# Kernel optimization log

Measured on AMD Instinct MI355X. Metric: run time of the kernel, lower is better.

The kernel has to match this reference:

```python
import jax, jax.numpy as jnp
import numpy as np

D_MODEL = 768
D_HEAD = 64
N_HEADS = D_MODEL // D_HEAD


def setup_inputs() -> dict:
    key = jax.random.key(0)
    k1, k2, k3 = jax.random.split(key, 3)
    n, h, w = 2, 48, 48
    x = jax.random.normal(k1, (n, h, w, D_MODEL), dtype=jnp.float32)
    # torch Linear weights: [out_features, in_features]
    w_qkv = jax.random.normal(k2, (3 * D_MODEL, D_MODEL), dtype=jnp.float32) * (D_MODEL ** -0.5)
    w_out = jax.random.normal(k3, (D_MODEL, D_MODEL), dtype=jnp.float32) * (D_MODEL ** -0.5)
    return {"x": x, "w_qkv": w_qkv, "w_out": w_out, "kernel_size": 7}


def _natten_mask(h: int, w: int, kernel_size: int) -> jnp.ndarray:
    # Faithful to _natten_mask_mod: q_x = idx // w, q_y = idx % w,
    # both axes compared against the same kernel_size.
    idx = jnp.arange(h * w)
    qx, qy = idx // w, idx % w
    horiz = jnp.abs(qx[:, None] - qx[None, :]) <= kernel_size
    vert = jnp.abs(qy[:, None] - qy[None, :]) <= kernel_size
    return horiz & vert  # [hw, hw] bool


def reference(x, w_qkv, w_out, kernel_size):
    n, h, w, d = x.shape
    hw = h * w
    qkv = jnp.einsum('nhwd,fd->nhwf', x, w_qkv)  # [n, h, w, 3*d]
    qkv = qkv.reshape(n, hw, 3, N_HEADS, D_HEAD)
    q = jnp.transpose(qkv[:, :, 0], (0, 2, 1, 3))  # [n, nh, hw, e]
    k = jnp.transpose(qkv[:, :, 1], (0, 2, 1, 3))
    v = jnp.transpose(qkv[:, :, 2], (0, 2, 1, 3))

    mask = _natten_mask(h, w, kernel_size)  # [hw, hw]
    scale = D_HEAD ** -0.5
    scores = jnp.einsum('bnqe,bnke->bnqk', q, k) * scale
    neg = jnp.asarray(jnp.finfo(scores.dtype).min, scores.dtype)
    scores = jnp.where(mask[None, None], scores, neg)
    attn = jax.nn.softmax(scores, axis=-1)
    o = jnp.einsum('bnqk,bnke->bnqe', attn, v)  # [n, nh, hw, e]
    o = jnp.transpose(o, (0, 2, 1, 3)).reshape(n, h, w, d)
    return jnp.einsum('nhwd,fd->nhwf', o, w_out)
```

## Files before the change

kernel.cpp:

```cpp
#include <hip/hip_runtime.h>

using f32x4 = __attribute__((ext_vector_type(4))) float;
using h8v   = __attribute__((ext_vector_type(8))) _Float16;
using h4v   = __attribute__((ext_vector_type(4))) _Float16;
using s8v   = __attribute__((ext_vector_type(8))) short;

#define MFMAH(a, b, c)   __builtin_amdgcn_mfma_f32_16x16x32_f16((a), (b), (c), 0, 0, 0)
#define MFMAH16(a, b, c) __builtin_amdgcn_mfma_f32_16x16x16f16((a), (b), (c), 0, 0, 0)

typedef __attribute__((address_space(3))) unsigned int lds_uint;
typedef const __attribute__((address_space(1))) unsigned int glb_uint;
__device__ inline void gload16(void* l, const void* g) {
    __builtin_amdgcn_global_load_lds((glb_uint*)g, (lds_uint*)l, 16, 0, 0);
}

__device__ inline float exp2_fast(float x) {
    float r;
    asm("v_exp_f32 %0, %1" : "=v"(r) : "v"(x));
    return r;
}

__global__ __launch_bounds__(256) void conv_all(const float* __restrict__ x,
                                                const float* __restrict__ wq,
                                                const float* __restrict__ wo,
                                                _Float16* __restrict__ xh,
                                                _Float16* __restrict__ wqh,
                                                _Float16* __restrict__ woh) {
    const int i = blockIdx.x * blockDim.x + threadIdx.x;
    const float* src;
    _Float16* dst;
    int off;
    if (i < 442368)      { src = x;  dst = xh;  off = i; }
    else if (i < 663552) { src = wq; dst = wqh; off = i - 442368; }
    else                 { src = wo; dst = woh; off = i - 663552; }
    const float4 a = *(const float4*)(src + (size_t)off * 8);
    const float4 b = *(const float4*)(src + (size_t)off * 8 + 4);
    h8v h;
    h[0] = (_Float16)a.x; h[1] = (_Float16)a.y; h[2] = (_Float16)a.z; h[3] = (_Float16)a.w;
    h[4] = (_Float16)b.x; h[5] = (_Float16)b.y; h[6] = (_Float16)b.z; h[7] = (_Float16)b.w;
    *(h8v*)(dst + (size_t)off * 8) = h;
}

__global__ __launch_bounds__(256) void gemm_qkv_f16(const _Float16* __restrict__ A,
                                                    const _Float16* __restrict__ B,
                                                    _Float16* __restrict__ C) {
    constexpr int LD = 768, LDC = 2304;
    __shared__ __align__(16) _Float16 sA[128][64], sB[128][64];
    const int b = blockIdx.x;
    const int sb = (b & 7) * 81 + (b >> 3);
    const int bx = sb % 18, by = sb / 18;
    const int m0 = by * 128, n0 = bx * 128;
    const int tid = threadIdx.x, lane = tid & 63, wv = tid >> 6;
    const int wm = (wv >> 1) * 64, wn = (wv & 1) * 64;
    const int fr = lane & 15, fkb = (lane >> 4) * 8;

    const int srow = tid >> 3, scol = (tid & 7) * 8;
    const _Float16* gA = A + (size_t)(m0 + srow) * LD + scol;
    const _Float16* gB = B + (size_t)(n0 + srow) * LD + scol;

    f32x4 acc[4][4];
#pragma unroll
    for (int m = 0; m < 4; ++m)
#pragma unroll
        for (int n2 = 0; n2 < 4; ++n2) acc[m][n2] = (f32x4){0.f, 0.f, 0.f, 0.f};

    for (int kt = 0; kt < 12; ++kt) {
        const int k0 = kt * 64;
#pragma unroll
        for (int q = 0; q < 4; ++q) {
            gload16(&sA[q * 32 + srow][scol], gA + (size_t)(q * 32) * LD + k0);
            gload16(&sB[q * 32 + srow][scol], gB + (size_t)(q * 32) * LD + k0);
        }
        __syncthreads();

#pragma unroll
        for (int kk = 0; kk < 2; ++kk) {
            h8v fa[4], fb[4];
#pragma unroll
            for (int m = 0; m < 4; ++m) fa[m] = *(const h8v*)&sA[wm + m * 16 + fr][kk * 32 + fkb];
#pragma unroll
            for (int n2 = 0; n2 < 4; ++n2) fb[n2] = *(const h8v*)&sB[wn + n2 * 16 + fr][kk * 32 + fkb];
#pragma unroll
            for (int m = 0; m < 4; ++m)
#pragma unroll
                for (int n2 = 0; n2 < 4; ++n2) acc[m][n2] = MFMAH(fa[m], fb[n2], acc[m][n2]);
        }
        __syncthreads();
    }

    const int rg = (lane >> 4) * 4;
#pragma unroll
    for (int m = 0; m < 4; ++m)
#pragma unroll
        for (int n2 = 0; n2 < 4; ++n2)
#pragma unroll
            for (int r = 0; r < 4; ++r)
                C[(size_t)(m0 + wm + m * 16 + rg + r) * LDC + (n0 + wn + n2 * 16 + fr)] =
                    (_Float16)acc[m][n2][r];
}

__global__ __launch_bounds__(256) void vtrans(const unsigned short* __restrict__ qkv,
                                              unsigned short* __restrict__ vt) {
    __shared__ unsigned short t[64][72];
    const int tt = blockIdx.x, head = blockIdx.y, n = blockIdx.z;
    const int tid = threadIdx.x;
#pragma unroll
    for (int i = 0; i < 2; ++i) {
        const int el = i * 2048 + tid * 8;
        const int tr = el >> 6, c = el & 63;
        s8v v = *(const s8v*)(qkv + (size_t)(n * 2304 + tt * 64 + tr) * 2304 + 1536 + head * 64 + c);
        *(s8v*)&t[tr][c] = v;
    }
    __syncthreads();
#pragma unroll
    for (int i = 0; i < 2; ++i) {
        const int el = i * 2048 + tid * 8;
        const int er = el >> 6, tk = el & 63;
        s8v w;
#pragma unroll
        for (int j = 0; j < 8; ++j) w[j] = (short)t[tk + j][er];
        *(s8v*)(vt + (size_t)((n * 12 + head) * 64 + er) * 2304 + tt * 64 + tk) = w;
    }
}

__global__ __launch_bounds__(192) void attn_flash(const _Float16* __restrict__ qkv,
                                                  const _Float16* __restrict__ vt,
                                                  _Float16* __restrict__ o,
                                                  const int* __restrict__ ksp) {
    __shared__ __align__(16) char sbuf[2][14336];
    const int tid = threadIdx.x;
    const int lane = tid & 63, wv = tid >> 6;
    const int fr = lane & 15, fg = lane >> 4;

    const int b = blockIdx.x;
    const int xcd = b & 7, g = b >> 3;
    const int qx = xcd * 6 + g / 24;
    const int hn = g % 24;
    const int head = hn >> 1, n = hn & 1;
    const int KS = *ksp;

    const int krow0 = tid >> 3, kc = tid & 7;
    const int vrow0 = tid / 6,  vc = tid % 6;
    const int ksw = (krow0 & 7) << 4;
    const int vsw = (vrow0 & 7) << 4;

    const int qy = wv * 16 + fr;
    const _Float16* qrow = qkv + (size_t)(n * 2304 + qx * 48 + qy) * 2304 + head * 64;
    h8v qa0 = *(const h8v*)(qrow + fg * 8);
    h8v qa1 = *(const h8v*)(qrow + 32 + fg * 8);
    qa0 = qa0 * (_Float16)0.1803368801f;
    qa1 = qa1 * (_Float16)0.1803368801f;

    int nt0 = (wv * 16 - KS) >> 4;      if (nt0 < 0) nt0 = 0;
    int nt1 = (wv * 16 + 15 + KS) >> 4; if (nt1 > 2) nt1 = 2;

    f32x4 mbias[3];
#pragma unroll
    for (int nt = 0; nt < 3; ++nt)
#pragma unroll
        for (int r = 0; r < 4; ++r) {
            const int dy = nt * 16 + fg * 4 + r - qy;
            mbias[nt][r] = (dy < -KS || dy > KS) ? -1e4f : 0.f;
        }

    f32x4 Oacc[4];
#pragma unroll
    for (int e = 0; e < 4; ++e) Oacc[e] = (f32x4){0.f, 0.f, 0.f, 0.f};
    float rs_acc = 0.f;

    const int lo = (qx - KS) > 0 ? (qx - KS) : 0;
    const int hi = (qx + KS) < 47 ? (qx + KS) : 47;

    const _Float16* kgbase = qkv + (size_t)(n * 2304) * 2304 + 768 + head * 64;
    const _Float16* vgbase = vt + (size_t)((n * 12 + head) * 64) * 2304;

    {
        const _Float16* kg = kgbase + (size_t)(lo * 48) * 2304;
        const _Float16* vg = vgbase + lo * 48;
        const s8v a0 = *(const s8v*)(kg + (size_t)krow0 * 2304 + kc * 8);
        const s8v a1 = *(const s8v*)(kg + (size_t)(krow0 + 24) * 2304 + kc * 8);
        const s8v b0 = *(const s8v*)(vg + (size_t)vrow0 * 2304 + vc * 8);
        const s8v b1 = *(const s8v*)(vg + (size_t)(vrow0 + 32) * 2304 + vc * 8);
        *(s8v*)(sbuf[0] + krow0 * 128 + ((kc * 16) ^ ksw)) = a0;
        *(s8v*)(sbuf[0] + (krow0 + 24) * 128 + ((kc * 16) ^ ksw)) = a1;
        *(s8v*)(sbuf[0] + 6144 + vrow0 * 128 + ((vc * 16) ^ vsw)) = b0;
        *(s8v*)(sbuf[0] + 6144 + (vrow0 + 32) * 128 + ((vc * 16) ^ vsw)) = b1;
    }

    int p = 0;
    for (int kx = lo; kx <= hi; ++kx) {
        __syncthreads();
        const bool pre = (kx < hi);
        s8v tk0, tk1, tv0, tv1;
        if (pre) {
            const _Float16* kg = kgbase + (size_t)((kx + 1) * 48) * 2304;
            const _Float16* vg = vgbase + (kx + 1) * 48;
            tk0 = *(const s8v*)(kg + (size_t)krow0 * 2304 + kc * 8);
            tk1 = *(const s8v*)(kg + (size_t)(krow0 + 24) * 2304 + kc * 8);
            tv0 = *(const s8v*)(vg + (size_t)vrow0 * 2304 + vc * 8);
            tv1 = *(const s8v*)(vg + (size_t)(vrow0 + 32) * 2304 + vc * 8);
        }

        const char* K = sbuf[p];
        const char* V = sbuf[p] + 6144;

        f32x4 s[3];
#pragma unroll
        for (int nt = 0; nt < 3; ++nt)
            if (nt >= nt0 && nt <= nt1) {
                const int rr = nt * 16 + fr;
                const int sw = (rr & 7) << 4;
                const h8v kb0 = *(const h8v*)(K + rr * 128 + ((fg * 16) ^ sw));
                const h8v kb1 = *(const h8v*)(K + rr * 128 + ((64 + fg * 16) ^ sw));
                f32x4 z = MFMAH(kb0, qa0, mbias[nt]);
                z = MFMAH(kb1, qa1, z);
                s[nt] = z;
            }

#pragma unroll
        for (int nt = 0; nt < 3; ++nt)
            if (nt >= nt0 && nt <= nt1) {
                h4v pa;
#pragma unroll
                for (int r = 0; r < 4; ++r) {
                    const float pv = exp2_fast(s[nt][r]);
                    rs_acc += pv;
                    pa[r] = (_Float16)pv;
                }
                const int slot = nt * 2 + (fg >> 1), off8 = (fg & 1) * 8;
#pragma unroll
                for (int et = 0; et < 4; ++et) {
                    const int rv = et * 16 + fr;
                    const h4v vb = *(const h4v*)(V + rv * 128 +
                                                 (((slot ^ (rv & 7)) << 4) + off8));
                    Oacc[et] = MFMAH16(vb, pa, Oacc[et]);
                }
            }

        if (pre) {
            char* d = sbuf[p ^ 1];
            *(s8v*)(d + krow0 * 128 + ((kc * 16) ^ ksw)) = tk0;
            *(s8v*)(d + (krow0 + 24) * 128 + ((kc * 16) ^ ksw)) = tk1;
            *(s8v*)(d + 6144 + vrow0 * 128 + ((vc * 16) ^ vsw)) = tv0;
            *(s8v*)(d + 6144 + (vrow0 + 32) * 128 + ((vc * 16) ^ vsw)) = tv1;
        }
        p ^= 1;
    }

    rs_acc += __shfl_xor(rs_acc, 16);
    rs_acc += __shfl_xor(rs_acc, 32);
    const float linv = 1.f / rs_acc;
    _Float16* ob = o + (size_t)(n * 2304 + qx * 48 + wv * 16 + fr) * 768 + head * 64;
#pragma unroll
    for (int et = 0; et < 4; ++et) {
        h4v ov;
#pragma unroll
        for (int r = 0; r < 4; ++r) ov[r] = (_Float16)(Oacc[et][r] * linv);
        *(h4v*)(ob + et * 16 + fg * 4) = ov;
    }
}

__global__ __launch_bounds__(256) void gemm_out_f16(const _Float16* __restrict__ A,
                                                    const _Float16* __restrict__ B,
                                                    float* __restrict__ C) {
    constexpr int LD = 768, LDC = 768;
    __shared__ __align__(16) _Float16 sA[128][64], sB[128][64];
    const int b = blockIdx.x;
    const int sb = (b & 7) * 27 + (b >> 3);
    const int bx = sb % 6, by = sb / 6;
    const int m0 = by * 128, n0 = bx * 128;
    const int tid = threadIdx.x, lane = tid & 63, wv = tid >> 6;
    const int wm = (wv >> 1) * 64, wn = (wv & 1) * 64;
    const int fr = lane & 15, fkb = (lane >> 4) * 8;

    const int srow = tid >> 3, scol = (tid & 7) * 8;
    const _Float16* gA = A + (size_t)(m0 + srow) * LD + scol;
    const _Float16* gB = B + (size_t)(n0 + srow) * LD + scol;

    f32x4 acc[4][4];
#pragma unroll
    for (int m = 0; m < 4; ++m)
#pragma unroll
        for (int n2 = 0; n2 < 4; ++n2) acc[m][n2] = (f32x4){0.f, 0.f, 0.f, 0.f};

    for (int kt = 0; kt < 12; ++kt) {
        const int k0 = kt * 64;
#pragma unroll
        for (int q = 0; q < 4; ++q) {
            gload16(&sA[q * 32 + srow][scol], gA + (size_t)(q * 32) * LD + k0);
            gload16(&sB[q * 32 + srow][scol], gB + (size_t)(q * 32) * LD + k0);
        }
        __syncthreads();

#pragma unroll
        for (int kk = 0; kk < 2; ++kk) {
            h8v fa[4], fb[4];
#pragma unroll
            for (int m = 0; m < 4; ++m) fa[m] = *(const h8v*)&sA[wm + m * 16 + fr][kk * 32 + fkb];
#pragma unroll
            for (int n2 = 0; n2 < 4; ++n2) fb[n2] = *(const h8v*)&sB[wn + n2 * 16 + fr][kk * 32 + fkb];
#pragma unroll
            for (int m = 0; m < 4; ++m)
#pragma unroll
                for (int n2 = 0; n2 < 4; ++n2) acc[m][n2] = MFMAH(fa[m], fb[n2], acc[m][n2]);
        }
        __syncthreads();
    }

    const int rg = (lane >> 4) * 4;
#pragma unroll
    for (int m = 0; m < 4; ++m)
#pragma unroll
        for (int n2 = 0; n2 < 4; ++n2)
#pragma unroll
            for (int r = 0; r < 4; ++r)
                C[(size_t)(m0 + wm + m * 16 + rg + r) * LDC + (n0 + wn + n2 * 16 + fr)] =
                    acc[m][n2][r];
}

extern "C" void kernel_launch(void* const* d_in, const int* in_sizes, int n_in,
                              void* d_out, int out_size, void* d_ws, size_t ws_size,
                              hipStream_t stream) {
    const float* x     = (const float*)d_in[0];
    const float* w_qkv = (const float*)d_in[1];
    const float* w_out = (const float*)d_in[2];
    const int*   ksp   = (const int*)d_in[3];
    float* out = (float*)d_out;

    char* ws = (char*)d_ws;
    _Float16* qkv = (_Float16*)(ws);
    _Float16* vt  = (_Float16*)(ws + 21237760);
    _Float16* o   = (_Float16*)(ws + 28315648);
    _Float16* xh  = (_Float16*)(ws + 35393536);
    _Float16* wqh = (_Float16*)(ws + 42471424);
    _Float16* woh = (_Float16*)(ws + 46010368);

    conv_all<<<dim3(2880), 256, 0, stream>>>(x, w_qkv, w_out, xh, wqh, woh);
    gemm_qkv_f16<<<dim3(648), 256, 0, stream>>>(xh, wqh, qkv);
    vtrans<<<dim3(36, 12, 2), 256, 0, stream>>>((const unsigned short*)qkv,
                                                (unsigned short*)vt);
    attn_flash<<<dim3(1152), 192, 0, stream>>>(qkv, vt, o, ksp);
    gemm_out_f16<<<dim3(216), 256, 0, stream>>>(o, woh, out);
}
```

Measured before the change: 86.73 us.

## Double-buffer GEMM K-tiles and share K/V loads across two query rows

Both GEMMs switch from a single 64-wide K tile to double-buffered 32-wide tiles, so the global→LDS async load of the next tile overlaps the MFMAs on the current one and one barrier per step is dropped. The attention kernel now uses 384-thread blocks covering two adjacent query rows. Each K/V row tile is loaded once and shared, and each wave skips rows outside its own window. This halves redundant K/V traffic per row pair, at the cost of some idle iterations per wave and larger blocks.

```diff
diff --git a/kernel.cpp b/kernel.cpp
--- a/kernel.cpp
+++ b/kernel.cpp
@@ -45,7 +45,7 @@
                                                     const _Float16* __restrict__ B,
                                                     _Float16* __restrict__ C) {
     constexpr int LD = 768, LDC = 2304;
-    __shared__ __align__(16) _Float16 sA[128][64], sB[128][64];
+    __shared__ __align__(16) _Float16 sA[2][128][32], sB[2][128][32];
     const int b = blockIdx.x;
     const int sb = (b & 7) * 81 + (b >> 3);
     const int bx = sb % 18, by = sb / 18;
@@ -54,7 +54,7 @@
     const int wm = (wv >> 1) * 64, wn = (wv & 1) * 64;
     const int fr = lane & 15, fkb = (lane >> 4) * 8;
 
-    const int srow = tid >> 3, scol = (tid & 7) * 8;
+    const int srow = tid >> 2, scol = (tid & 3) * 8;
     const _Float16* gA = A + (size_t)(m0 + srow) * LD + scol;
     const _Float16* gB = B + (size_t)(n0 + srow) * LD + scol;
 
@@ -64,28 +64,33 @@
 #pragma unroll
         for (int n2 = 0; n2 < 4; ++n2) acc[m][n2] = (f32x4){0.f, 0.f, 0.f, 0.f};
 
-    for (int kt = 0; kt < 12; ++kt) {
-        const int k0 = kt * 64;
-#pragma unroll
-        for (int q = 0; q < 4; ++q) {
-            gload16(&sA[q * 32 + srow][scol], gA + (size_t)(q * 32) * LD + k0);
-            gload16(&sB[q * 32 + srow][scol], gB + (size_t)(q * 32) * LD + k0);
-        }
+    gload16(&sA[0][srow][scol],      gA);
+    gload16(&sA[0][64 + srow][scol], gA + 64 * LD);
+    gload16(&sB[0][srow][scol],      gB);
+    gload16(&sB[0][64 + srow][scol], gB + 64 * LD);
+
+    int cur = 0;
+    for (int kt = 0; kt < 24; ++kt) {
+        asm volatile("s_waitcnt vmcnt(0)" ::: "memory");
         __syncthreads();
-
-#pragma unroll
-        for (int kk = 0; kk < 2; ++kk) {
-            h8v fa[4], fb[4];
-#pragma unroll
-            for (int m = 0; m < 4; ++m) fa[m] = *(const h8v*)&sA[wm + m * 16 + fr][kk * 32 + fkb];
-#pragma unroll
-            for (int n2 = 0; n2 < 4; ++n2) fb[n2] = *(const h8v*)&sB[wn + n2 * 16 + fr][kk * 32 + fkb];
-#pragma unroll
-            for (int m = 0; m < 4; ++m)
-#pragma unroll
-                for (int n2 = 0; n2 < 4; ++n2) acc[m][n2] = MFMAH(fa[m], fb[n2], acc[m][n2]);
-        }
-        __syncthreads();
+        if (kt + 1 < 24) {
+            const int k1 = (kt + 1) * 32;
+            gload16(&sA[cur ^ 1][srow][scol],      gA + k1);
+            gload16(&sA[cur ^ 1][64 + srow][scol], gA + 64 * LD + k1);
+            gload16(&sB[cur ^ 1][srow][scol],      gB + k1);
+            gload16(&sB[cur ^ 1][64 + srow][scol], gB + 64 * LD + k1);
+        }
+
+        h8v fa[4], fb[4];
+#pragma unroll
+        for (int m = 0; m < 4; ++m) fa[m] = *(const h8v*)&sA[cur][wm + m * 16 + fr][fkb];
+#pragma unroll
+        for (int n2 = 0; n2 < 4; ++n2) fb[n2] = *(const h8v*)&sB[cur][wn + n2 * 16 + fr][fkb];
+#pragma unroll
+        for (int m = 0; m < 4; ++m)
+#pragma unroll
+            for (int n2 = 0; n2 < 4; ++n2) acc[m][n2] = MFMAH(fa[m], fb[n2], acc[m][n2]);
+        cur ^= 1;
     }
 
     const int rg = (lane >> 4) * 4;
@@ -123,26 +128,28 @@
     }
 }
 
-__global__ __launch_bounds__(192) void attn_flash(const _Float16* __restrict__ qkv,
+__global__ __launch_bounds__(384) void attn_flash(const _Float16* __restrict__ qkv,
                                                   const _Float16* __restrict__ vt,
                                                   _Float16* __restrict__ o,
                                                   const int* __restrict__ ksp) {
     __shared__ __align__(16) char sbuf[2][14336];
     const int tid = threadIdx.x;
-    const int lane = tid & 63, wv = tid >> 6;
+    const int lane = tid & 63, w = tid >> 6;
     const int fr = lane & 15, fg = lane >> 4;
 
     const int b = blockIdx.x;
     const int xcd = b & 7, g = b >> 3;
-    const int qx = xcd * 6 + g / 24;
+    const int qxp = xcd * 3 + g / 24;
     const int hn = g % 24;
     const int head = hn >> 1, n = hn & 1;
+    const int qxl = w / 3, wv = w % 3;
+    const int qx = qxp * 2 + qxl;
     const int KS = *ksp;
 
-    const int krow0 = tid >> 3, kc = tid & 7;
-    const int vrow0 = tid / 6,  vc = tid % 6;
-    const int ksw = (krow0 & 7) << 4;
-    const int vsw = (vrow0 & 7) << 4;
+    const int krow = tid >> 3, kc = tid & 7;
+    const int vrow = tid / 6,  vc = tid % 6;
+    const int ksw = (krow & 7) << 4;
+    const int vsw = (vrow & 7) << 4;
 
     const int qy = wv * 16 + fr;
     const _Float16* qrow = qkv + (size_t)(n * 2304 + qx * 48 + qy) * 2304 + head * 64;
@@ -168,81 +175,72 @@
     for (int e = 0; e < 4; ++e) Oacc[e] = (f32x4){0.f, 0.f, 0.f, 0.f};
     float rs_acc = 0.f;
 
-    const int lo = (qx - KS) > 0 ? (qx - KS) : 0;
-    const int hi = (qx + KS) < 47 ? (qx + KS) : 47;
+    const int lo = (2 * qxp - KS) > 0 ? (2 * qxp - KS) : 0;
+    const int hi = (2 * qxp + 1 + KS) < 47 ? (2 * qxp + 1 + KS) : 47;
+    const int wlo = qx - KS, whi = qx + KS;
 
     const _Float16* kgbase = qkv + (size_t)(n * 2304) * 2304 + 768 + head * 64;
     const _Float16* vgbase = vt + (size_t)((n * 12 + head) * 64) * 2304;
 
     {
-        const _Float16* kg = kgbase + (size_t)(lo * 48) * 2304;
-        const _Float16* vg = vgbase + lo * 48;
-        const s8v a0 = *(const s8v*)(kg + (size_t)krow0 * 2304 + kc * 8);
-        const s8v a1 = *(const s8v*)(kg + (size_t)(krow0 + 24) * 2304 + kc * 8);
-        const s8v b0 = *(const s8v*)(vg + (size_t)vrow0 * 2304 + vc * 8);
-        const s8v b1 = *(const s8v*)(vg + (size_t)(vrow0 + 32) * 2304 + vc * 8);
-        *(s8v*)(sbuf[0] + krow0 * 128 + ((kc * 16) ^ ksw)) = a0;
-        *(s8v*)(sbuf[0] + (krow0 + 24) * 128 + ((kc * 16) ^ ksw)) = a1;
-        *(s8v*)(sbuf[0] + 6144 + vrow0 * 128 + ((vc * 16) ^ vsw)) = b0;
-        *(s8v*)(sbuf[0] + 6144 + (vrow0 + 32) * 128 + ((vc * 16) ^ vsw)) = b1;
+        const s8v a0 = *(const s8v*)(kgbase + (size_t)(lo * 48 + krow) * 2304 + kc * 8);
+        const s8v b0 = *(const s8v*)(vgbase + (size_t)vrow * 2304 + lo * 48 + vc * 8);
+        *(s8v*)(sbuf[0] + krow * 128 + ((kc * 16) ^ ksw)) = a0;
+        *(s8v*)(sbuf[0] + 6144 + vrow * 128 + ((vc * 16) ^ vsw)) = b0;
     }
 
     int p = 0;
     for (int kx = lo; kx <= hi; ++kx) {
         __syncthreads();
         const bool pre = (kx < hi);
-        s8v tk0, tk1, tv0, tv1;
+        s8v tk, tv;
         if (pre) {
-            const _Float16* kg = kgbase + (size_t)((kx + 1) * 48) * 2304;
-            const _Float16* vg = vgbase + (kx + 1) * 48;
-            tk0 = *(const s8v*)(kg + (size_t)krow0 * 2304 + kc * 8);
-            tk1 = *(const s8v*)(kg + (size_t)(krow0 + 24) * 2304 + kc * 8);
-            tv0 = *(const s8v*)(vg + (size_t)vrow0 * 2304 + vc * 8);
-            tv1 = *(const s8v*)(vg + (size_t)(vrow0 + 32) * 2304 + vc * 8);
-        }
-
-        const char* K = sbuf[p];
-        const char* V = sbuf[p] + 6144;
-
-        f32x4 s[3];
-#pragma unroll
-        for (int nt = 0; nt < 3; ++nt)
-            if (nt >= nt0 && nt <= nt1) {
-                const int rr = nt * 16 + fr;
-                const int sw = (rr & 7) << 4;
-                const h8v kb0 = *(const h8v*)(K + rr * 128 + ((fg * 16) ^ sw));
-                const h8v kb1 = *(const h8v*)(K + rr * 128 + ((64 + fg * 16) ^ sw));
-                f32x4 z = MFMAH(kb0, qa0, mbias[nt]);
-                z = MFMAH(kb1, qa1, z);
-                s[nt] = z;
-            }
-
-#pragma unroll
-        for (int nt = 0; nt < 3; ++nt)
-            if (nt >= nt0 && nt <= nt1) {
-                h4v pa;
-#pragma unroll
-                for (int r = 0; r < 4; ++r) {
-                    const float pv = exp2_fast(s[nt][r]);
-                    rs_acc += pv;
-                    pa[r] = (_Float16)pv;
+            tk = *(const s8v*)(kgbase + (size_t)((kx + 1) * 48 + krow) * 2304 + kc * 8);
+            tv = *(const s8v*)(vgbase + (size_t)vrow * 2304 + (kx + 1) * 48 + vc * 8);
+        }
+
+        if (kx >= wlo && kx <= whi) {
+            const char* K = sbuf[p];
+            const char* V = sbuf[p] + 6144;
+
+            f32x4 s[3];
+#pragma unroll
+            for (int nt = 0; nt < 3; ++nt)
+                if (nt >= nt0 && nt <= nt1) {
+                    const int rr = nt * 16 + fr;
+                    const int sw = (rr & 7) << 4;
+                    const h8v kb0 = *(const h8v*)(K + rr * 128 + ((fg * 16) ^ sw));
+                    const h8v kb1 = *(const h8v*)(K + rr * 128 + ((64 + fg * 16) ^ sw));
+                    f32x4 z = MFMAH(kb0, qa0, mbias[nt]);
+                    z = MFMAH(kb1, qa1, z);
+                    s[nt] = z;
                 }
-                const int slot = nt * 2 + (fg >> 1), off8 = (fg & 1) * 8;
-#pragma unroll
-                for (int et = 0; et < 4; ++et) {
-                    const int rv = et * 16 + fr;
-                    const h4v vb = *(const h4v*)(V + rv * 128 +
-                                                 (((slot ^ (rv & 7)) << 4) + off8));
-                    Oacc[et] = MFMAH16(vb, pa, Oacc[et]);
+
+#pragma unroll
+            for (int nt = 0; nt < 3; ++nt)
+                if (nt >= nt0 && nt <= nt1) {
+                    h4v pa;
+#pragma unroll
+                    for (int r = 0; r < 4; ++r) {
+                        const float pv = exp2_fast(s[nt][r]);
+                        rs_acc += pv;
+                        pa[r] = (_Float16)pv;
+                    }
+                    const int slot = nt * 2 + (fg >> 1), off8 = (fg & 1) * 8;
+#pragma unroll
+                    for (int et = 0; et < 4; ++et) {
+                        const int rv = et * 16 + fr;
+                        const h4v vb = *(const h4v*)(V + rv * 128 +
+                                                     (((slot ^ (rv & 7)) << 4) + off8));
+                        Oacc[et] = MFMAH16(vb, pa, Oacc[et]);
+                    }
                 }
-            }
+        }
 
         if (pre) {
             char* d = sbuf[p ^ 1];
-            *(s8v*)(d + krow0 * 128 + ((kc * 16) ^ ksw)) = tk0;
-            *(s8v*)(d + (krow0 + 24) * 128 + ((kc * 16) ^ ksw)) = tk1;
-            *(s8v*)(d + 6144 + vrow0 * 128 + ((vc * 16) ^ vsw)) = tv0;
-            *(s8v*)(d + 6144 + (vrow0 + 32) * 128 + ((vc * 16) ^ vsw)) = tv1;
+            *(s8v*)(d + krow * 128 + ((kc * 16) ^ ksw)) = tk;
+            *(s8v*)(d + 6144 + vrow * 128 + ((vc * 16) ^ vsw)) = tv;
         }
         p ^= 1;
     }
@@ -264,7 +262,7 @@
                                                     const _Float16* __restrict__ B,
                                                     float* __restrict__ C) {
     constexpr int LD = 768, LDC = 768;
-    __shared__ __align__(16) _Float16 sA[128][64], sB[128][64];
+    __shared__ __align__(16) _Float16 sA[2][128][32], sB[2][128][32];
     const int b = blockIdx.x;
     const int sb = (b & 7) * 27 + (b >> 3);
     const int bx = sb % 6, by = sb / 6;
@@ -273,7 +271,7 @@
     const int wm = (wv >> 1) * 64, wn = (wv & 1) * 64;
     const int fr = lane & 15, fkb = (lane >> 4) * 8;
 
-    const int srow = tid >> 3, scol = (tid & 7) * 8;
+    const int srow = tid >> 2, scol = (tid & 3) * 8;
     const _Float16* gA = A + (size_t)(m0 + srow) * LD + scol;
     const _Float16* gB = B + (size_t)(n0 + srow) * LD + scol;
 
@@ -283,28 +281,33 @@
 #pragma unroll
         for (int n2 = 0; n2 < 4; ++n2) acc[m][n2] = (f32x4){0.f, 0.f, 0.f, 0.f};
 
-    for (int kt = 0; kt < 12; ++kt) {
-        const int k0 = kt * 64;
-#pragma unroll
-        for (int q = 0; q < 4; ++q) {
-            gload16(&sA[q * 32 + srow][scol], gA + (size_t)(q * 32) * LD + k0);
-            gload16(&sB[q * 32 + srow][scol], gB + (size_t)(q * 32) * LD + k0);
-        }
+    gload16(&sA[0][srow][scol],      gA);
+    gload16(&sA[0][64 + srow][scol], gA + 64 * LD);
+    gload16(&sB[0][srow][scol],      gB);
+    gload16(&sB[0][64 + srow][scol], gB + 64 * LD);
+
+    int cur = 0;
+    for (int kt = 0; kt < 24; ++kt) {
+        asm volatile("s_waitcnt vmcnt(0)" ::: "memory");
         __syncthreads();
-
-#pragma unroll
-        for (int kk = 0; kk < 2; ++kk) {
-            h8v fa[4], fb[4];
-#pragma unroll
-            for (int m = 0; m < 4; ++m) fa[m] = *(const h8v*)&sA[wm + m * 16 + fr][kk * 32 + fkb];
-#pragma unroll
-            for (int n2 = 0; n2 < 4; ++n2) fb[n2] = *(const h8v*)&sB[wn + n2 * 16 + fr][kk * 32 + fkb];
-#pragma unroll
-            for (int m = 0; m < 4; ++m)
-#pragma unroll
-                for (int n2 = 0; n2 < 4; ++n2) acc[m][n2] = MFMAH(fa[m], fb[n2], acc[m][n2]);
-        }
-        __syncthreads();
+        if (kt + 1 < 24) {
+            const int k1 = (kt + 1) * 32;
+            gload16(&sA[cur ^ 1][srow][scol],      gA + k1);
+            gload16(&sA[cur ^ 1][64 + srow][scol], gA + 64 * LD + k1);
+            gload16(&sB[cur ^ 1][srow][scol],      gB + k1);
+            gload16(&sB[cur ^ 1][64 + srow][scol], gB + 64 * LD + k1);
+        }
+
+        h8v fa[4], fb[4];
+#pragma unroll
+        for (int m = 0; m < 4; ++m) fa[m] = *(const h8v*)&sA[cur][wm + m * 16 + fr][fkb];
+#pragma unroll
+        for (int n2 = 0; n2 < 4; ++n2) fb[n2] = *(const h8v*)&sB[cur][wn + n2 * 16 + fr][fkb];
+#pragma unroll
+        for (int m = 0; m < 4; ++m)
+#pragma unroll
+            for (int n2 = 0; n2 < 4; ++n2) acc[m][n2] = MFMAH(fa[m], fb[n2], acc[m][n2]);
+        cur ^= 1;
     }
 
     const int rg = (lane >> 4) * 4;
@@ -339,6 +342,6 @@
     gemm_qkv_f16<<<dim3(648), 256, 0, stream>>>(xh, wqh, qkv);
     vtrans<<<dim3(36, 12, 2), 256, 0, stream>>>((const unsigned short*)qkv,
                                                 (unsigned short*)vt);
-    attn_flash<<<dim3(1152), 192, 0, stream>>>(qkv, vt, o, ksp);
+    attn_flash<<<dim3(576), 384, 0, stream>>>(qkv, vt, o, ksp);
     gemm_out_f16<<<dim3(216), 256, 0, stream>>>(o, woh, out);
 }
```

Result: slower. 94.32 us (+8.7%).
